# Optimization experiments

Hardware: AMD Instinct MI355X
Metric: run time of the kernel (lower is better)

## Reference

```python
import jax, jax.numpy as jnp
import numpy as np

KNOTS = 17
T_MAX = 3.0


def _trapezoid(knots=KNOTS, t_max=T_MAX):
    t = jnp.linspace(0.0, t_max, knots, dtype=jnp.float32)
    dt = t_max / (knots - 1)
    w = jnp.full((knots,), 2.0 * dt, dtype=jnp.float32)
    w = w.at[0].set(dt).at[-1].set(dt)
    weights = w * jnp.exp(-t * t / 2.0)
    return t, weights


def setup_inputs() -> dict:
    key = jax.random.key(0)
    k1, k2 = jax.random.split(key)
    z = jax.random.normal(k1, (32, 128, 512), dtype=jnp.float32)   # (T, B, D)
    A = jax.random.normal(k2, (512, 1024), dtype=jnp.float32)      # (D, M) raw, normalized inside
    return {"z": z, "A": A}


def reference(z, A):
    t, weights = _trapezoid()                       # (K,), (K,)
    # column-normalize random projections (matches A / A.norm(dim=0).clamp_min(1e-12))
    norm = jnp.sqrt(jnp.sum(A * A, axis=0, keepdims=True))
    An = A / jnp.maximum(norm, 1e-12)
    proj = jnp.einsum('tbd,dm->tbm', z, An)         # (T, B, M)
    xt = proj[..., None] * t                        # (T, B, M, K) — dominant intermediate
    cos_mean = jnp.mean(jnp.cos(xt), axis=1)        # reduce over B -> (T, M, K)
    sin_mean = jnp.mean(jnp.sin(xt), axis=1)
    target = jnp.exp(-t * t / 2.0)                  # (K,)
    err = (cos_mean - target) ** 2 + sin_mean ** 2  # (T, M, K)
    statistic = err @ weights                       # (T, M)
    statistic = statistic * z.shape[1]              # multiply by B (proj.size(-2))
    return jnp.mean(statistic)
```

## Files before the change

### kernel.cpp

```cpp
#include <hip/hip_runtime.h>
#include <hip/hip_bf16.h>
#include <math.h>

#define T_DIM 32
#define B_DIM 128
#define D_DIM 512
#define M_DIM 1024

constexpr float DT = 0.1875f;
constexpr float INV_2PI = 0.15915494309189535f;

typedef __attribute__((ext_vector_type(8))) short bf16x8;
typedef __attribute__((ext_vector_type(4))) float f32x4;
typedef __attribute__((ext_vector_type(2))) float f32x2;

__device__ __forceinline__ ushort f2bf(float f) {
    unsigned u = __float_as_uint(f);
    u += 0x7FFFu + ((u >> 16) & 1u);
    return (ushort)(u >> 16);
}

__device__ __forceinline__ void gload16(const void* g, void* l) {
    __builtin_amdgcn_global_load_lds(
        (const __attribute__((address_space(1))) void*)g,
        (__attribute__((address_space(3))) void*)l, 16, 0, 0);
}

__device__ __forceinline__ void fast_sincos(float theta, float& s, float& c) {
    float r = theta * INV_2PI;
    r -= floorf(r);
    s = __builtin_amdgcn_sinf(r);
    c = __builtin_amdgcn_cosf(r);
}

__global__ __launch_bounds__(256) void prep_kernel(const float* __restrict__ A,
                                                   const float* __restrict__ z,
                                                   ushort* __restrict__ zb,
                                                   ushort* __restrict__ ant) {
    const int bid = blockIdx.x;
    const int tid = threadIdx.x;

    if (bid >= 64) {
        const size_t base = (size_t)(bid - 64) * 8192 + tid * 8;
#pragma unroll
        for (int j = 0; j < 4; ++j) {
            const size_t i = base + j * 2048;
            const float4 a = *reinterpret_cast<const float4*>(&z[i]);
            const float4 b = *reinterpret_cast<const float4*>(&z[i + 4]);
            uint4 p;
            p.x = (unsigned)f2bf(a.x) | ((unsigned)f2bf(a.y) << 16);
            p.y = (unsigned)f2bf(a.z) | ((unsigned)f2bf(a.w) << 16);
            p.z = (unsigned)f2bf(b.x) | ((unsigned)f2bf(b.y) << 16);
            p.w = (unsigned)f2bf(b.z) | ((unsigned)f2bf(b.w) << 16);
            *reinterpret_cast<uint4*>(&zb[i]) = p;
        }
        return;
    }

    __shared__ float red[256];
    __shared__ float inv[16];
    __shared__ float tile[128][17];

    const int mB = bid * 16;
    const int mo = tid & 15;
    const int dg = tid >> 4;
    float ss = 0.0f;
#pragma unroll 4
    for (int i = 0; i < 32; ++i) {
        const float v = A[(size_t)(dg * 32 + i) * M_DIM + mB + mo];
        ss = fmaf(v, v, ss);
    }
    red[tid] = ss;
    __syncthreads();
    for (int s = 128; s >= 16; s >>= 1) {
        if (tid < s) red[tid] += red[tid + s];
        __syncthreads();
    }
    if (tid < 16) inv[tid] = 1.0f / fmaxf(sqrtf(red[tid]), 1e-12f);

#pragma unroll
    for (int ch = 0; ch < 4; ++ch) {
        const int dB = ch * 128;
#pragma unroll
        for (int q = 0; q < 2; ++q) {
            const int s  = tid + 256 * q;
            const int r  = s >> 2;
            const int c4 = (s & 3) * 4;
            const float4 v = *reinterpret_cast<const float4*>(
                &A[(size_t)(dB + r) * M_DIM + mB + c4]);
            tile[r][c4]     = v.x;
            tile[r][c4 + 1] = v.y;
            tile[r][c4 + 2] = v.z;
            tile[r][c4 + 3] = v.w;
        }
        __syncthreads();
        {
            const int m  = tid >> 4;
            const int d8 = (tid & 15) * 8;
            const float sc = inv[m];
            uint4 p;
            p.x = (unsigned)f2bf(tile[d8 + 0][m] * sc) | ((unsigned)f2bf(tile[d8 + 1][m] * sc) << 16);
            p.y = (unsigned)f2bf(tile[d8 + 2][m] * sc) | ((unsigned)f2bf(tile[d8 + 3][m] * sc) << 16);
            p.z = (unsigned)f2bf(tile[d8 + 4][m] * sc) | ((unsigned)f2bf(tile[d8 + 5][m] * sc) << 16);
            p.w = (unsigned)f2bf(tile[d8 + 6][m] * sc) | ((unsigned)f2bf(tile[d8 + 7][m] * sc) << 16);
            *reinterpret_cast<uint4*>(&ant[(size_t)(mB + m) * D_DIM + dB + d8]) = p;
        }
        __syncthreads();
    }
}

#define CHEB(CS) { const f32x2 nxt = c2 * cur - prev; prev = cur; cur = nxt; CS += cur; }
#define CF_ALL(V) { \
    float s1, c1; fast_sincos((V) * DT, s1, c1); \
    const float c2 = 2.0f * c1; \
    f32x2 prev = {1.0f, 0.0f}; \
    f32x2 cur  = {c1, s1}; \
    cs0 += cur; \
    CHEB(cs1)  CHEB(cs2)  CHEB(cs3)  CHEB(cs4)  CHEB(cs5) \
    CHEB(cs6)  CHEB(cs7)  CHEB(cs8)  CHEB(cs9)  CHEB(cs10) \
    CHEB(cs11) CHEB(cs12) CHEB(cs13) CHEB(cs14) CHEB(cs15) }
#define RED(CS) { \
    CS.x += __shfl_xor(CS.x, 16); CS.x += __shfl_xor(CS.x, 32); \
    CS.y += __shfl_xor(CS.y, 16); CS.y += __shfl_xor(CS.y, 32); }
#define ST(CS, K) { wred[wc][l15][K] = CS.x; wred[wc][l15][16 + K] = CS.y; }
#define FIN(CS, KK) { \
    constexpr float tk = DT * (float)(KK); \
    const float g  = __expf(-0.5f * tk * tk); \
    const float w  = (((KK) == 16) ? DT : 2.0f * DT) * g; \
    const float totC = wred[wc][l15][(KK) - 1]      + CS.x; \
    const float totS = wred[wc][l15][16 + (KK) - 1] + CS.y; \
    const float cm = fmaf(totC, invB, -g); \
    const float sm = totS * invB; \
    s = fmaf(w, fmaf(cm, cm, sm * sm), s); }

__global__ __launch_bounds__(256) void fused_kernel(const ushort* __restrict__ zb,
                                                    const ushort* __restrict__ ant,
                                                    float* __restrict__ partials) {
    __shared__ __align__(16) ushort As[128 * 64];
    __shared__ __align__(16) ushort Bs[32 * 64];
    __shared__ float wred[2][16][33];
    __shared__ float bred[2];

    const int tid  = threadIdx.x;
    const int mB   = blockIdx.x * 32;
    const int t    = blockIdx.y;
    const int wave = tid >> 6;
    const int lane = tid & 63;
    const int wr   = wave >> 1;
    const int wc   = wave & 1;
    const int l15  = lane & 15;
    const int lhi  = lane >> 4;

    const int l8 = lane >> 3;
    const int cx = ((lane & 7) ^ l8) * 8;

    const ushort* zrow = zb + (size_t)t * B_DIM * D_DIM;

    f32x4 acc[4];
#pragma unroll
    for (int fm = 0; fm < 4; ++fm) acc[fm] = (f32x4)(0.0f);

    const int swz = (l15 & 7) * 8;

#pragma unroll
    for (int it = 0; it < 8; ++it) {
        const int k0 = it * 64;
#pragma unroll
        for (int j = 0; j < 4; ++j) {
            const int r0 = wave * 32 + j * 8;
            gload16(&zrow[(size_t)(r0 + l8) * D_DIM + k0 + cx], &As[r0 * 64]);
        }
        {
            const int r0 = wave * 8;
            gload16(&ant[(size_t)(mB + r0 + l8) * D_DIM + k0 + cx], &Bs[r0 * 64]);
        }
        __syncthreads();

#pragma unroll
        for (int ks = 0; ks < 2; ++ks) {
            const int co = (ks * 32 + lhi * 8) ^ swz;
            const bf16x8 bfrag = *reinterpret_cast<const bf16x8*>(&Bs[(wc * 16 + l15) * 64 + co]);
#pragma unroll
            for (int fm = 0; fm < 4; ++fm) {
                const bf16x8 afrag = *reinterpret_cast<const bf16x8*>(&As[(wr * 64 + fm * 16 + l15) * 64 + co]);
                acc[fm] = __builtin_amdgcn_mfma_f32_16x16x32_bf16(afrag, bfrag, acc[fm], 0, 0, 0);
            }
        }
        __syncthreads();
    }

    f32x2 cs0  = {0.f, 0.f}, cs1  = {0.f, 0.f}, cs2  = {0.f, 0.f}, cs3  = {0.f, 0.f};
    f32x2 cs4  = {0.f, 0.f}, cs5  = {0.f, 0.f}, cs6  = {0.f, 0.f}, cs7  = {0.f, 0.f};
    f32x2 cs8  = {0.f, 0.f}, cs9  = {0.f, 0.f}, cs10 = {0.f, 0.f}, cs11 = {0.f, 0.f};
    f32x2 cs12 = {0.f, 0.f}, cs13 = {0.f, 0.f}, cs14 = {0.f, 0.f}, cs15 = {0.f, 0.f};

#pragma unroll
    for (int fm = 0; fm < 4; ++fm) {
        const f32x4 av = acc[fm];
        CF_ALL(av.x) CF_ALL(av.y) CF_ALL(av.z) CF_ALL(av.w)
    }

    RED(cs0)  RED(cs1)  RED(cs2)  RED(cs3)  RED(cs4)  RED(cs5)  RED(cs6)  RED(cs7)
    RED(cs8)  RED(cs9)  RED(cs10) RED(cs11) RED(cs12) RED(cs13) RED(cs14) RED(cs15)

    if (wr == 0 && lane < 16) {
        ST(cs0, 0)   ST(cs1, 1)   ST(cs2, 2)   ST(cs3, 3)
        ST(cs4, 4)   ST(cs5, 5)   ST(cs6, 6)   ST(cs7, 7)
        ST(cs8, 8)   ST(cs9, 9)   ST(cs10, 10) ST(cs11, 11)
        ST(cs12, 12) ST(cs13, 13) ST(cs14, 14) ST(cs15, 15)
    }
    __syncthreads();

    if (wr == 1) {
        const float invB = 1.0f / 128.0f;
        float s = 0.0f;
        FIN(cs0, 1)   FIN(cs1, 2)   FIN(cs2, 3)   FIN(cs3, 4)
        FIN(cs4, 5)   FIN(cs5, 6)   FIN(cs6, 7)   FIN(cs7, 8)
        FIN(cs8, 9)   FIN(cs9, 10)  FIN(cs10, 11) FIN(cs11, 12)
        FIN(cs12, 13) FIN(cs13, 14) FIN(cs14, 15) FIN(cs15, 16)
#pragma unroll
        for (int m = 1; m < 64; m <<= 1) s += __shfl_xor(s, m);
        if (lane == 0) bred[wc] = s;
    }
    __syncthreads();
    if (tid == 0)
        partials[blockIdx.y * 32 + blockIdx.x] = bred[0] + bred[1];
}

__global__ __launch_bounds__(256) void finalize_kernel(const float* __restrict__ partials,
                                                       float* __restrict__ out) {
    __shared__ float red[256];
    const int tid = threadIdx.x;
    red[tid] = partials[tid] + partials[tid + 256] + partials[tid + 512] + partials[tid + 768];
    __syncthreads();
    for (int s = 128; s > 0; s >>= 1) {
        if (tid < s) red[tid] += red[tid + s];
        __syncthreads();
    }
    if (tid == 0) out[0] = red[0] * (1.0f / 1024.0f);
}

extern "C" void kernel_launch(void* const* d_in, const int* in_sizes, int n_in,
                              void* d_out, int out_size, void* d_ws, size_t ws_size,
                              hipStream_t stream) {
    const float* z = (const float*)d_in[0];
    const float* A = (const float*)d_in[1];
    float* out = (float*)d_out;

    char* ws = (char*)d_ws;
    ushort* zb       = (ushort*)ws;
    ushort* ant      = (ushort*)(ws + 4 * 1024 * 1024);
    float*  partials = (float*)(ws + 5 * 1024 * 1024);

    prep_kernel<<<320, 256, 0, stream>>>(A, z, zb, ant);
    fused_kernel<<<dim3(M_DIM / 32, T_DIM), 256, 0, stream>>>(zb, ant, partials);
    finalize_kernel<<<1, 256, 0, stream>>>(partials, out);
}
```

Measured before the change: 32.19 us.

## Double K-tile to 128, re-swizzle LDS, union reduction buffers, spread z conversion

The GEMM main loop now stages 128-wide K tiles, which halves the iteration count and the number of barriers. It uses a new 16-way XOR swizzle, and the epilogue reduction arrays share LDS with the A tile through a union. The bf16 conversion of z in the prep kernel is split across twice as many blocks, each doing half the work, to raise parallelism. LDS use per block grows, which may reduce occupancy.

```diff
diff --git a/kernel.cpp b/kernel.cpp
--- a/kernel.cpp
+++ b/kernel.cpp
@@ -41,9 +41,9 @@
     const int tid = threadIdx.x;
 
     if (bid >= 64) {
-        const size_t base = (size_t)(bid - 64) * 8192 + tid * 8;
-#pragma unroll
-        for (int j = 0; j < 4; ++j) {
+        const size_t base = (size_t)(bid - 64) * 4096 + tid * 8;
+#pragma unroll
+        for (int j = 0; j < 2; ++j) {
             const size_t i = base + j * 2048;
             const float4 a = *reinterpret_cast<const float4*>(&z[i]);
             const float4 b = *reinterpret_cast<const float4*>(&z[i + 4]);
@@ -136,10 +136,11 @@
 __global__ __launch_bounds__(256) void fused_kernel(const ushort* __restrict__ zb,
                                                     const ushort* __restrict__ ant,
                                                     float* __restrict__ partials) {
-    __shared__ __align__(16) ushort As[128 * 64];
-    __shared__ __align__(16) ushort Bs[32 * 64];
-    __shared__ float wred[2][16][33];
-    __shared__ float bred[2];
+    __shared__ __align__(16) union SharedU {
+        ushort As[128 * 128];
+        struct { float wred[2][16][33]; float bred[2]; } r;
+    } u;
+    __shared__ __align__(16) ushort Bs[32 * 128];
 
     const int tid  = threadIdx.x;
     const int mB   = blockIdx.x * 32;
@@ -151,8 +152,8 @@
     const int l15  = lane & 15;
     const int lhi  = lane >> 4;
 
-    const int l8 = lane >> 3;
-    const int cx = ((lane & 7) ^ l8) * 8;
+    const int rofs = lane >> 4;
+    const int gl   = lane & 15;
 
     const ushort* zrow = zb + (size_t)t * B_DIM * D_DIM;
 
@@ -160,34 +161,41 @@
 #pragma unroll
     for (int fm = 0; fm < 4; ++fm) acc[fm] = (f32x4)(0.0f);
 
-    const int swz = (l15 & 7) * 8;
-
-#pragma unroll
-    for (int it = 0; it < 8; ++it) {
-        const int k0 = it * 64;
-#pragma unroll
-        for (int j = 0; j < 4; ++j) {
-            const int r0 = wave * 32 + j * 8;
-            gload16(&zrow[(size_t)(r0 + l8) * D_DIM + k0 + cx], &As[r0 * 64]);
-        }
-        {
-            const int r0 = wave * 8;
-            gload16(&ant[(size_t)(mB + r0 + l8) * D_DIM + k0 + cx], &Bs[r0 * 64]);
-        }
-        __syncthreads();
-
-#pragma unroll
-        for (int ks = 0; ks < 2; ++ks) {
-            const int co = (ks * 32 + lhi * 8) ^ swz;
-            const bf16x8 bfrag = *reinterpret_cast<const bf16x8*>(&Bs[(wc * 16 + l15) * 64 + co]);
+#pragma unroll
+    for (int it = 0; it < 4; ++it) {
+        const int k0 = it * 128;
+#pragma unroll
+        for (int j = 0; j < 8; ++j) {
+            const int r0  = wave * 32 + j * 4;
+            const int row = r0 + rofs;
+            const int gs  = gl ^ (row & 15);
+            gload16(&zrow[(size_t)row * D_DIM + k0 + gs * 8], &u.As[r0 * 128]);
+        }
+#pragma unroll
+        for (int j = 0; j < 2; ++j) {
+            const int r0  = wave * 8 + j * 4;
+            const int row = r0 + rofs;
+            const int gs  = gl ^ (row & 15);
+            gload16(&ant[(size_t)(mB + row) * D_DIM + k0 + gs * 8], &Bs[r0 * 128]);
+        }
+        __syncthreads();
+
+#pragma unroll
+        for (int ks = 0; ks < 4; ++ks) {
+            const int gd = (ks * 4 + lhi) ^ l15;
+            const int co = gd * 8;
+            const bf16x8 bfrag = *reinterpret_cast<const bf16x8*>(&Bs[(wc * 16 + l15) * 128 + co]);
 #pragma unroll
             for (int fm = 0; fm < 4; ++fm) {
-                const bf16x8 afrag = *reinterpret_cast<const bf16x8*>(&As[(wr * 64 + fm * 16 + l15) * 64 + co]);
+                const bf16x8 afrag = *reinterpret_cast<const bf16x8*>(&u.As[(wr * 64 + fm * 16 + l15) * 128 + co]);
                 acc[fm] = __builtin_amdgcn_mfma_f32_16x16x32_bf16(afrag, bfrag, acc[fm], 0, 0, 0);
             }
         }
         __syncthreads();
     }
+
+    float (&wred)[2][16][33] = u.r.wred;
+    float (&bred)[2] = u.r.bred;
 
     f32x2 cs0  = {0.f, 0.f}, cs1  = {0.f, 0.f}, cs2  = {0.f, 0.f}, cs3  = {0.f, 0.f};
     f32x2 cs4  = {0.f, 0.f}, cs5  = {0.f, 0.f}, cs6  = {0.f, 0.f}, cs7  = {0.f, 0.f};
@@ -252,7 +260,7 @@
     ushort* ant      = (ushort*)(ws + 4 * 1024 * 1024);
     float*  partials = (float*)(ws + 5 * 1024 * 1024);
 
-    prep_kernel<<<320, 256, 0, stream>>>(A, z, zb, ant);
+    prep_kernel<<<576, 256, 0, stream>>>(A, z, zb, ant);
     fused_kernel<<<dim3(M_DIM / 32, T_DIM), 256, 0, stream>>>(zb, ant, partials);
     finalize_kernel<<<1, 256, 0, stream>>>(partials, out);
 }
```

Measured after the change: 31.59 us. About the same (-1.8%).
